# Kernel optimization log

Hardware: AMD Instinct MI355X
Metric: run time of the kernel (lower is better)

## Reference

```python
import jax, jax.numpy as jnp
import numpy as np

NB_HEAD = 12
INPUT_DIM = 768
HEAD_DIM = INPUT_DIM // NB_HEAD


def setup_inputs() -> dict:
    key = jax.random.key(0)
    kx, kq, kv = jax.random.split(key, 3)
    x = jax.random.normal(kx, (32, 512, INPUT_DIM), dtype=jnp.float32)
    # per-head params stacked on a leading head axis; original init: uniform(-0.1, 0.1)
    Q = jax.random.uniform(kq, (NB_HEAD, INPUT_DIM, INPUT_DIM), dtype=jnp.float32, minval=-0.1, maxval=0.1)
    V = jax.random.uniform(kv, (NB_HEAD, INPUT_DIM, HEAD_DIM), dtype=jnp.float32, minval=-0.1, maxval=0.1)
    return {"x": x, "Q": Q, "V": V}


def reference(x, Q, V):
    # x: [b, n, d]; Q: [h, d, d]; V: [h, d, e] with e = head_dim
    b, n, d = x.shape
    h = Q.shape[0]
    q = jnp.einsum('bnd,hde->bhne', x, Q)            # per-head query proj
    scores = jnp.einsum('bhne,bme->bhnm', q, x)      # QK^T with raw x as keys (no scaling)
    att = jax.nn.softmax(scores, axis=-1)            # softmax over keys
    weighted = jnp.einsum('bhnm,bmd->bhnd', att, x)  # attention-weighted values (raw x)
    out = jnp.einsum('bhnd,hde->bhne', weighted, V)  # per-head output proj
    # concat heads along feature dim (head 0 first, matching torch.cat)
    return out.transpose(0, 2, 1, 3).reshape(b, n, h * V.shape[-1])
```

## Files before the change

### kernel.cpp

```cpp
#include <hip/hip_runtime.h>
#include <stdint.h>

#define B_SZ 32
#define SEQ  512
#define DIM  768
#define NH   12
#define HD   64
#define ROWS (B_SZ*SEQ)

typedef __attribute__((ext_vector_type(4))) float f32x4;
typedef __attribute__((ext_vector_type(8))) _Float16 half8;

#define GLOAD_LDS16(gaddr, laddr) \
  __builtin_amdgcn_global_load_lds((const __attribute__((address_space(1))) void*)(gaddr), \
                                   (__attribute__((address_space(3))) void*)(laddr), 16, 0, 0)

__device__ __forceinline__ unsigned short h2u(_Float16 h){
  union { _Float16 h; unsigned short u; } c; c.h = h; return c.u;
}
__device__ __forceinline__ unsigned short f2hu(float f){
  return h2u((_Float16)f);
}

__global__ void k_split(const float* __restrict__ x,
                        unsigned short* __restrict__ xh,
                        unsigned short* __restrict__ xl, int n4){
  int i = blockIdx.x * 256 + threadIdx.x;
  if (i >= n4) return;
  float4 v = ((const float4*)x)[i];
  ushort4 h, l;
  _Float16 t;
  t = (_Float16)v.x; h.x = h2u(t); l.x = f2hu(v.x - (float)t);
  t = (_Float16)v.y; h.y = h2u(t); l.y = f2hu(v.y - (float)t);
  t = (_Float16)v.z; h.z = h2u(t); l.z = f2hu(v.z - (float)t);
  t = (_Float16)v.w; h.w = h2u(t); l.w = f2hu(v.w - (float)t);
  ((ushort4*)xh)[i] = h;
  ((ushort4*)xl)[i] = l;
}

__global__ __launch_bounds__(256) void k_transQ(const float* __restrict__ Q,
                         unsigned short* __restrict__ qth,
                         unsigned short* __restrict__ qtl){
  __shared__ float tile[32][33];
  int h = blockIdx.z;
  int d0 = blockIdx.x * 32;
  int e0 = blockIdx.y * 32;
  int tx = threadIdx.x & 31, ty = threadIdx.x >> 5;
  const float* Qh = Q + (size_t)h * DIM * DIM;
  for (int i = 0; i < 4; ++i)
    tile[ty + i*8][tx] = Qh[(size_t)(d0 + ty + i*8) * DIM + e0 + tx];
  __syncthreads();
  for (int i = 0; i < 4; ++i){
    float v = tile[tx][ty + i*8];
    size_t o = ((size_t)h * DIM + e0 + ty + i*8) * DIM + d0 + tx;
    _Float16 hi = (_Float16)v;
    qth[o] = h2u(hi);
    qtl[o] = f2hu(v - (float)hi);
  }
}

__global__ __launch_bounds__(256) void k_transV(const float* __restrict__ V,
                         unsigned short* __restrict__ vt16){
  __shared__ float tile[32][33];
  int h = blockIdx.z;
  int d0 = blockIdx.x * 32;
  int e0 = blockIdx.y * 32;
  int tx = threadIdx.x & 31, ty = threadIdx.x >> 5;
  const float* Vh = V + (size_t)h * DIM * HD;
  for (int i = 0; i < 4; ++i)
    tile[ty + i*8][tx] = Vh[(size_t)(d0 + ty + i*8) * HD + e0 + tx];
  __syncthreads();
  for (int i = 0; i < 4; ++i)
    vt16[((size_t)h * HD + e0 + ty + i*8) * DIM + d0 + tx] = f2hu(tile[tx][ty + i*8]);
}

__global__ __launch_bounds__(256) void k_gemm_xv(
    const unsigned short* __restrict__ xh,
    const unsigned short* __restrict__ vt16,
    unsigned short* __restrict__ xvT){
  __shared__ __align__(16) unsigned short lA[128*32];
  __shared__ __align__(16) unsigned short lB[64*32];
  __shared__ __align__(16) unsigned short lOut[64*128];
  int t = threadIdx.x, w = t >> 6, l = t & 63;
  int lane16 = l & 15, quad = l >> 4;
  int b = blockIdx.y, h = blockIdx.z;
  int m0 = blockIdx.x * 128;
  const unsigned short* vth = vt16 + (size_t)h * HD * DIM;
  f32x4 acc[2][4];
  for (int i = 0; i < 2; ++i) for (int j = 0; j < 4; ++j)
    for (int z = 0; z < 4; ++z) acc[i][j][z] = 0.f;

  for (int kt = 0; kt < DIM/32; ++kt){
    int k0 = kt * 32;
    __syncthreads();
    for (int rep = 0; rep < 2; ++rep){
      int id = t + rep * 256;
      int row = id >> 2, ko = (id & 3) * 8;
      GLOAD_LDS16(&xh[((size_t)(b*SEQ + m0 + row))*DIM + k0 + ko],
                  &lA[(rep*256 + w*64) * 8]);
    }
    { int row = t >> 2, ko = (t & 3) * 8;
      GLOAD_LDS16(&vth[(size_t)row*DIM + k0 + ko], &lB[(w*64) * 8]); }
    __syncthreads();
    half8 a[2];
    for (int i = 0; i < 2; ++i)
      a[i] = *(const half8*)&lA[(w*32 + i*16 + lane16)*32 + quad*8];
    for (int j = 0; j < 4; ++j){
      half8 bb = *(const half8*)&lB[(j*16 + lane16)*32 + quad*8];
      for (int i = 0; i < 2; ++i)
        acc[i][j] = __builtin_amdgcn_mfma_f32_16x16x32_f16(a[i], bb, acc[i][j], 0, 0, 0);
    }
  }
  __syncthreads();
  for (int i = 0; i < 2; ++i) for (int j = 0; j < 4; ++j) for (int r = 0; r < 4; ++r){
    int col = j*16 + lane16;
    int n  = w*32 + i*16 + quad*4 + r;
    lOut[col*128 + n] = f2hu(acc[i][j][r]);
  }
  __syncthreads();
  for (int rep = 0; rep < 4; ++rep){
    int id = t + rep*256;
    int e = id >> 4, no = (id & 15) * 8;
    *(int4*)&xvT[((size_t)(b*NH + h)*HD + e)*SEQ + m0 + no] = *(const int4*)&lOut[e*128 + no];
  }
}

__global__ __launch_bounds__(256, 2) void k_gemm_q(
    const unsigned short* __restrict__ xh, const unsigned short* __restrict__ xl,
    const unsigned short* __restrict__ bth, const unsigned short* __restrict__ btl,
    unsigned short* __restrict__ qh, unsigned short* __restrict__ ql, int ncols){
  __shared__ __align__(16) unsigned short lA[2][128*64];
  __shared__ __align__(16) unsigned short lB[2][128*64];
  int t = threadIdx.x, w = t >> 6, l = t & 63;
  int lane16 = l & 15, quad = l >> 4;
  int m0 = blockIdx.x * 128, n0 = blockIdx.y * 128;
  int wr = (w >> 1) * 64, wc = (w & 1) * 64;
  f32x4 acc[4][4];
  for (int i = 0; i < 4; ++i) for (int j = 0; j < 4; ++j)
    for (int z = 0; z < 4; ++z) acc[i][j][z] = 0.f;

  for (int kt = 0; kt < DIM/64; ++kt){
    int k0 = kt * 64;
    __syncthreads();
    for (int rep = 0; rep < 4; ++rep){
      int id = t + rep * 256;
      int row = id >> 3;
      int gc  = (id & 7) ^ (row & 7);
      int lb  = (rep*256 + w*64) * 8;
      size_t gA = (size_t)(m0+row)*DIM + k0 + gc*8;
      size_t gB = (size_t)(n0+row)*DIM + k0 + gc*8;
      GLOAD_LDS16(&xh [gA], &lA[0][lb]);
      GLOAD_LDS16(&xl [gA], &lA[1][lb]);
      GLOAD_LDS16(&bth[gB], &lB[0][lb]);
      GLOAD_LDS16(&btl[gB], &lB[1][lb]);
    }
    __syncthreads();
    for (int ks = 0; ks < 2; ++ks){
      int sw = ((ks*4 + quad) ^ (lane16 & 7)) * 8;
      half8 aH[4], aL[4];
      for (int i = 0; i < 4; ++i){
        int r = wr + i*16 + lane16;
        aH[i] = *(const half8*)&lA[0][r*64 + sw];
        aL[i] = *(const half8*)&lA[1][r*64 + sw];
      }
      for (int j = 0; j < 4; ++j){
        int c = wc + j*16 + lane16;
        half8 bH = *(const half8*)&lB[0][c*64 + sw];
        half8 bL = *(const half8*)&lB[1][c*64 + sw];
        for (int i = 0; i < 4; ++i){
          acc[i][j] = __builtin_amdgcn_mfma_f32_16x16x32_f16(aL[i], bH, acc[i][j], 0, 0, 0);
          acc[i][j] = __builtin_amdgcn_mfma_f32_16x16x32_f16(aH[i], bL, acc[i][j], 0, 0, 0);
          acc[i][j] = __builtin_amdgcn_mfma_f32_16x16x32_f16(aH[i], bH, acc[i][j], 0, 0, 0);
        }
      }
    }
  }
  for (int i = 0; i < 4; ++i) for (int j = 0; j < 4; ++j) for (int r = 0; r < 4; ++r){
    int row = m0 + wr + i*16 + quad*4 + r;
    int col = n0 + wc + j*16 + lane16;
    float v = acc[i][j][r];
    _Float16 hh = (_Float16)v;
    size_t o = (size_t)row*ncols + col;
    qh[o] = h2u(hh);
    ql[o] = f2hu(v - (float)hh);
  }
}

#define SEQP 520
__global__ __launch_bounds__(512) void k_attn(
    const unsigned short* __restrict__ qh, const unsigned short* __restrict__ ql,
    const unsigned short* __restrict__ xh, const unsigned short* __restrict__ xl,
    const unsigned short* __restrict__ xvT,
    float* __restrict__ out, int h0, int hc){
  __shared__ __align__(16) unsigned short lsh[73728];
  __shared__ float lStat[8*64 + 64 + 64];

  int t = threadIdx.x, w = t >> 6, l = t & 63;
  int lane16 = l & 15, quad = l >> 4;
  int bx = blockIdx.x, b = blockIdx.y;
  int hIdx = bx % hc, nt = bx / hc;
  int h = h0 + hIdx;
  int qstride = hc * 768;
  size_t qoff = (size_t)hIdx * 768;
  int n0 = nt * 64;
  size_t rowbase = (size_t)b * SEQ;
  const size_t dQ = (size_t)(ql - qh);
  const size_t dX = (size_t)(xl - xh);

  f32x4 accS[4][4];
  for (int i = 0; i < 4; ++i) for (int j = 0; j < 4; ++j)
    for (int z = 0; z < 4; ++z) accS[i][j][z] = 0.f;

  auto stage = [&](int kt){
    int k0 = kt * 32, bb = kt & 1;
    int qb = 65536 + bb*4096;
    {
      int row = t >> 3, s = t & 7, c = s ^ (row & 7);
      size_t hilo = (size_t)(c >> 2);
      GLOAD_LDS16(&qh[(rowbase + n0 + row)*qstride + qoff + k0 + (c & 3)*8 + hilo*dQ],
                  &lsh[qb + t*8]);
    }
    int kb = bb*32768;
    for (int rep = 0; rep < 8; ++rep){
      int id = t + rep * 512;
      int row = id >> 3, s = id & 7, c = s ^ (row & 7);
      size_t hilo = (size_t)(c >> 2);
      GLOAD_LDS16(&xh[(rowbase + row)*DIM + k0 + (c & 3)*8 + hilo*dX],
                  &lsh[kb + id*8]);
    }
  };

  stage(0);
  for (int kt = 0; kt < DIM/32; ++kt){
    __syncthreads();
    if (kt + 1 < DIM/32) stage(kt + 1);
    int bb = kt & 1;
    int qb = 65536 + bb*4096, kb = bb*32768;
    half8 aH[4], aL[4];
    for (int i = 0; i < 4; ++i){
      int r = i*16 + lane16;
      aH[i] = *(const half8*)&lsh[qb + r*64 + (( quad    ^ (r & 7))*8)];
      aL[i] = *(const half8*)&lsh[qb + r*64 + (((quad+4) ^ (r & 7))*8)];
    }
    for (int j = 0; j < 4; ++j){
      int c = w*64 + j*16 + lane16;
      half8 bH = *(const half8*)&lsh[kb + c*64 + (( quad    ^ (c & 7))*8)];
      half8 bL = *(const half8*)&lsh[kb + c*64 + (((quad+4) ^ (c & 7))*8)];
      for (int i = 0; i < 4; ++i){
        accS[i][j] = __builtin_amdgcn_mfma_f32_16x16x32_f16(aL[i], bH, accS[i][j], 0, 0, 0);
        accS[i][j] = __builtin_amdgcn_mfma_f32_16x16x32_f16(aH[i], bL, accS[i][j], 0, 0, 0);
        accS[i][j] = __builtin_amdgcn_mfma_f32_16x16x32_f16(aH[i], bH, accS[i][j], 0, 0, 0);
      }
    }
  }
  __syncthreads();

  const int XVB = 34816;
  for (int it = 0; it < 8; ++it){
    int e = it*8 + w;
    GLOAD_LDS16(&xvT[((size_t)(b*NH + h)*HD + e)*SEQ + l*8], &lsh[XVB + e*SEQP]);
  }

  float rmx[4][4];
  for (int i = 0; i < 4; ++i) for (int r = 0; r < 4; ++r){
    float m = accS[i][0][r];
    for (int j = 1; j < 4; ++j) m = fmaxf(m, accS[i][j][r]);
    for (int d = 1; d < 16; d <<= 1) m = fmaxf(m, __shfl_xor(m, d, 64));
    rmx[i][r] = m;
  }
  if (lane16 == 0)
    for (int i = 0; i < 4; ++i) for (int r = 0; r < 4; ++r)
      lStat[w*64 + i*16 + quad*4 + r] = rmx[i][r];
  __syncthreads();
  if (t < 64){
    float m = lStat[t];
    for (int ww = 1; ww < 8; ++ww) m = fmaxf(m, lStat[ww*64 + t]);
    lStat[512 + t] = m;
  }
  __syncthreads();
  float rsum[4][4];
  for (int i = 0; i < 4; ++i) for (int r = 0; r < 4; ++r){
    float g = lStat[512 + i*16 + quad*4 + r];
    float s = 0.f;
    for (int j = 0; j < 4; ++j){
      float p = __expf(accS[i][j][r] - g);
      s += p;
      lsh[(i*16 + quad*4 + r)*SEQP + (w*64 + j*16 + lane16)] = f2hu(p);
    }
    for (int d = 1; d < 16; d <<= 1) s += __shfl_xor(s, d, 64);
    rsum[i][r] = s;
  }
  if (lane16 == 0)
    for (int i = 0; i < 4; ++i) for (int r = 0; r < 4; ++r)
      lStat[w*64 + i*16 + quad*4 + r] = rsum[i][r];
  __syncthreads();
  if (t < 64){
    float s = lStat[t];
    for (int ww = 1; ww < 8; ++ww) s += lStat[ww*64 + t];
    lStat[576 + t] = s;
  }
  __syncthreads();

  f32x4 accO[4][4];
  for (int i = 0; i < 4; ++i) for (int j = 0; j < 4; ++j)
    for (int z = 0; z < 4; ++z) accO[i][j][z] = 0.f;
  for (int ks = 0; ks < 2; ++ks){
    int kb = w*64 + ks*32;
    half8 aP[4];
    for (int i = 0; i < 4; ++i)
      aP[i] = *(const half8*)&lsh[(i*16 + lane16)*SEQP + kb + quad*8];
    for (int j = 0; j < 4; ++j){
      half8 bV = *(const half8*)&lsh[XVB + (j*16 + lane16)*SEQP + kb + quad*8];
      for (int i = 0; i < 4; ++i)
        accO[i][j] = __builtin_amdgcn_mfma_f32_16x16x32_f16(aP[i], bV, accO[i][j], 0, 0, 0);
    }
  }
  __syncthreads();
  float* red = (float*)lsh;
  for (int i = 0; i < 4; ++i) for (int j = 0; j < 4; ++j) for (int r = 0; r < 4; ++r)
    red[w*4096 + (i*16 + quad*4 + r)*64 + (j*16 + lane16)] = accO[i][j][r];
  __syncthreads();
  for (int z = t; z < 4096; z += 512){
    int row = z >> 6, col = z & 63;
    float v = 0.f;
    for (int ww = 0; ww < 8; ++ww) v += red[ww*4096 + z];
    v /= lStat[576 + row];
    out[(rowbase + n0 + row)*DIM + h*HD + col] = v;
  }
}

extern "C" void kernel_launch(void* const* d_in, const int* in_sizes, int n_in,
                              void* d_out, int out_size, void* d_ws, size_t ws_size,
                              hipStream_t stream){
  const float* x = (const float*)d_in[0];
  const float* Q = (const float*)d_in[1];
  const float* V = (const float*)d_in[2];
  float* out = (float*)d_out;

  char* ws = (char*)d_ws;
  size_t off = 0;
  auto alloc = [&](size_t bytes) -> void* {
    void* p = ws + off;
    off += (bytes + 255) & ~(size_t)255;
    return p;
  };
  unsigned short* xh  = (unsigned short*)alloc((size_t)ROWS*DIM*2);
  unsigned short* xl  = (unsigned short*)alloc((size_t)ROWS*DIM*2);
  unsigned short* qth = (unsigned short*)alloc((size_t)NH*DIM*DIM*2);
  unsigned short* qtl = (unsigned short*)alloc((size_t)NH*DIM*DIM*2);
  unsigned short* vt  = (unsigned short*)alloc((size_t)NH*HD*DIM*2);
  unsigned short* xvT = (unsigned short*)alloc((size_t)B_SZ*NH*HD*SEQ*2);

  const int hcands[6] = {12, 6, 4, 3, 2, 1};
  int HC = 1;
  for (int i = 0; i < 6; ++i){
    size_t qb_bytes = ((size_t)ROWS * hcands[i] * DIM * 2 + 255) & ~(size_t)255;
    if (off + 2*qb_bytes <= ws_size){ HC = hcands[i]; break; }
  }
  unsigned short* qbh = (unsigned short*)alloc((size_t)ROWS*HC*DIM*2);
  unsigned short* qbl = (unsigned short*)alloc((size_t)ROWS*HC*DIM*2);

  int n4 = ROWS*DIM/4;
  k_split<<<n4/256, 256, 0, stream>>>(x, xh, xl, n4);
  k_transQ<<<dim3(DIM/32, DIM/32, NH), 256, 0, stream>>>(Q, qth, qtl);
  k_transV<<<dim3(DIM/32, HD/32, NH), 256, 0, stream>>>(V, vt);
  k_gemm_xv<<<dim3(4, B_SZ, NH), 256, 0, stream>>>(xh, vt, xvT);

  for (int h0 = 0; h0 < NH; h0 += HC){
    k_gemm_q<<<dim3(ROWS/128, HC*DIM/128), 256, 0, stream>>>(
        xh, xl, qth + (size_t)h0*DIM*DIM, qtl + (size_t)h0*DIM*DIM,
        qbh, qbl, HC*DIM);
    k_attn<<<dim3(8*HC, B_SZ), 512, 0, stream>>>(
        qbh, qbl, xh, xl, xvT, out, h0, HC);
  }
}
```

Baseline: 1.558 ms.

## Give each wave private K tiles and register-load Q to remove per-step barriers

The QK^T loop in k_attn used to stage the Q tile and the shared K tile in LDS, with a block-wide __syncthreads every k-step. Now each wave loads only its own 64 K rows into a private LDS region, and Q fragments are read from global memory straight into registers, double-buffered across two k-steps. Ordering is enforced with manual s_waitcnt vmcnt instead of barriers. This is meant to remove the per-iteration barrier and the Q round trip through LDS. In exchange, Q is reloaded redundantly by all 8 waves, register pressure rises, and the hand-counted vmcnt values are fragile.

```diff
diff --git a/kernel.cpp b/kernel.cpp
--- a/kernel.cpp
+++ b/kernel.cpp
@@ -200,8 +200,8 @@
   int bx = blockIdx.x, b = blockIdx.y;
   int hIdx = bx % hc, nt = bx / hc;
   int h = h0 + hIdx;
-  int qstride = hc * 768;
-  size_t qoff = (size_t)hIdx * 768;
+  int qstride = hc * DIM;
+  size_t qoff = (size_t)hIdx * DIM;
   int n0 = nt * 64;
   size_t rowbase = (size_t)b * SEQ;
   const size_t dQ = (size_t)(ql - qh);
@@ -211,47 +211,56 @@
   for (int i = 0; i < 4; ++i) for (int j = 0; j < 4; ++j)
     for (int z = 0; z < 4; ++z) accS[i][j][z] = 0.f;
 
-  auto stage = [&](int kt){
-    int k0 = kt * 32, bb = kt & 1;
-    int qb = 65536 + bb*4096;
-    {
-      int row = t >> 3, s = t & 7, c = s ^ (row & 7);
-      size_t hilo = (size_t)(c >> 2);
-      GLOAD_LDS16(&qh[(rowbase + n0 + row)*qstride + qoff + k0 + (c & 3)*8 + hilo*dQ],
-                  &lsh[qb + t*8]);
-    }
-    int kb = bb*32768;
+  auto stageK = [&](int kt){
+    int k0 = kt * 32;
+    int base = (kt & 1)*32768 + w*4096;
     for (int rep = 0; rep < 8; ++rep){
-      int id = t + rep * 512;
+      int id = rep*64 + l;
       int row = id >> 3, s = id & 7, c = s ^ (row & 7);
       size_t hilo = (size_t)(c >> 2);
-      GLOAD_LDS16(&xh[(rowbase + row)*DIM + k0 + (c & 3)*8 + hilo*dX],
-                  &lsh[kb + id*8]);
+      GLOAD_LDS16(&xh[(rowbase + w*64 + row)*DIM + k0 + (c & 3)*8 + hilo*dX],
+                  &lsh[base + id*8]);
     }
   };
-
-  stage(0);
-  for (int kt = 0; kt < DIM/32; ++kt){
-    __syncthreads();
-    if (kt + 1 < DIM/32) stage(kt + 1);
-    int bb = kt & 1;
-    int qb = 65536 + bb*4096, kb = bb*32768;
-    half8 aH[4], aL[4];
+  auto loadQ = [&](int kt, half8* aH, half8* aL){
+    int k0 = kt * 32;
     for (int i = 0; i < 4; ++i){
-      int r = i*16 + lane16;
-      aH[i] = *(const half8*)&lsh[qb + r*64 + (( quad    ^ (r & 7))*8)];
-      aL[i] = *(const half8*)&lsh[qb + r*64 + (((quad+4) ^ (r & 7))*8)];
-    }
+      size_t o = (rowbase + n0 + i*16 + lane16)*(size_t)qstride + qoff + k0 + quad*8;
+      aH[i] = *(const half8*)&qh[o];
+      aL[i] = *(const half8*)&qh[o + dQ];
+    }
+  };
+  auto computeS = [&](int kt, half8* aH, half8* aL){
+    int kbase = (kt & 1)*32768 + w*4096;
     for (int j = 0; j < 4; ++j){
-      int c = w*64 + j*16 + lane16;
-      half8 bH = *(const half8*)&lsh[kb + c*64 + (( quad    ^ (c & 7))*8)];
-      half8 bL = *(const half8*)&lsh[kb + c*64 + (((quad+4) ^ (c & 7))*8)];
+      int r = j*16 + lane16;
+      half8 bH = *(const half8*)&lsh[kbase + r*64 + (( quad    ^ (r & 7))*8)];
+      half8 bL = *(const half8*)&lsh[kbase + r*64 + (((quad+4) ^ (r & 7))*8)];
       for (int i = 0; i < 4; ++i){
         accS[i][j] = __builtin_amdgcn_mfma_f32_16x16x32_f16(aL[i], bH, accS[i][j], 0, 0, 0);
         accS[i][j] = __builtin_amdgcn_mfma_f32_16x16x32_f16(aH[i], bL, accS[i][j], 0, 0, 0);
         accS[i][j] = __builtin_amdgcn_mfma_f32_16x16x32_f16(aH[i], bH, accS[i][j], 0, 0, 0);
       }
     }
+  };
+
+  half8 aH0[4], aL0[4], aH1[4], aL1[4];
+  stageK(0);
+  asm volatile("" ::: "memory");
+  loadQ(0, aH0, aL0);
+  for (int kt = 0; kt < DIM/32; kt += 2){
+    asm volatile("s_waitcnt vmcnt(8)" ::: "memory");
+    stageK(kt + 1);
+    asm volatile("" ::: "memory");
+    loadQ(kt + 1, aH1, aL1);
+    computeS(kt, aH0, aL0);
+    asm volatile("s_waitcnt vmcnt(8)" ::: "memory");
+    if (kt + 2 < DIM/32){
+      stageK(kt + 2);
+      asm volatile("" ::: "memory");
+      loadQ(kt + 2, aH0, aL0);
+    }
+    computeS(kt + 1, aH1, aL1);
   }
   __syncthreads();
 
```

New measurement: 1.877 ms. +20.5%, slower.
